# Performance work log

Hardware: AMD Instinct MI355X
Metric: run time of the kernel (lower is better)

Reference implementation:

```python
import jax, jax.numpy as jnp
import numpy as np

N_NODES = 50000


def _gcn_conv(h, W, b, src, dst, dinv):
    # PyG GCNConv: linear transform, then symmetric-normalized sum aggregation
    h = h @ W  # (N, d_out)
    norm = dinv[src] * dinv[dst]  # (E,)
    msg = h[src] * norm[:, None]  # (E, d_out)
    agg = jax.ops.segment_sum(msg, dst, num_segments=N_NODES)
    return agg + b


def setup_inputs() -> dict:
    key = jax.random.key(0)
    ks = jax.random.split(key, 9)
    in_dim, h1, h2, out_dim = 512, 512, 512, 256
    x = jax.random.normal(ks[0], (N_NODES, in_dim), dtype=jnp.float32)
    edge_index = jax.random.randint(ks[1], (2, 800000), 0, N_NODES, dtype=jnp.int64)

    def glorot(k, shape):
        lim = float(np.sqrt(6.0 / (shape[0] + shape[1])))
        return jax.random.uniform(k, shape, jnp.float32, -lim, lim)

    return {
        "x": x,
        "edge_index": edge_index,
        "W1": glorot(ks[2], (in_dim, h1)),
        "b1": jnp.zeros((h1,), jnp.float32),
        "W2": glorot(ks[3], (h1, h2)),
        "b2": jnp.zeros((h2,), jnp.float32),
        "Wout": glorot(ks[4], (h2, out_dim)),
        "bout": jnp.zeros((out_dim,), jnp.float32),
    }


def reference(x, edge_index, W1, b1, W2, b2, Wout, bout):
    # add self-loops (GCNConv default)
    loop = jnp.arange(N_NODES, dtype=edge_index.dtype)
    src = jnp.concatenate([edge_index[0], loop])
    dst = jnp.concatenate([edge_index[1], loop])
    # degree on A + I (target side), deg^{-1/2}
    deg = jax.ops.segment_sum(jnp.ones_like(dst, dtype=x.dtype), dst, num_segments=N_NODES)
    dinv = jnp.where(deg > 0, jax.lax.rsqrt(deg), 0.0)

    h = jax.nn.relu(_gcn_conv(x, W1, b1, src, dst, dinv))
    h = jax.nn.relu(_gcn_conv(h, W2, b2, src, dst, dinv))
    return h @ Wout + bout
```

## Files before the change

kernel.cpp:

```cpp
#include <hip/hip_runtime.h>

#define NN 50000
#define MP 50048
#define DD 512
#define EE 800000
#define NSCAN 196

typedef unsigned short u16;
typedef __attribute__((ext_vector_type(4))) float f32x4;
typedef __attribute__((ext_vector_type(8))) __bf16 bf16x8;
typedef __attribute__((ext_vector_type(8))) short s16x8;
typedef __attribute__((ext_vector_type(4))) short s16x4;

typedef __attribute__((address_space(1))) const void GVoid;
typedef __attribute__((address_space(3))) void LVoid;

__device__ __forceinline__ u16 f2bf(float f) {
  union { float f; unsigned u; } x; x.f = f;
  unsigned r = x.u + 0x7fffu + ((x.u >> 16) & 1u);
  return (u16)(r >> 16);
}
__device__ __forceinline__ float bf2f(u16 b) {
  union { unsigned u; float f; } x; x.u = ((unsigned)b) << 16;
  return x.f;
}


__global__ __launch_bounds__(256) void init_cnt_k(int* cnt) {
  int i = blockIdx.x * 256 + threadIdx.x;
  if (i < NN) cnt[i] = 1;
}

__global__ __launch_bounds__(256) void count_k(const int* __restrict__ dst, int* __restrict__ cnt) {
  int e = blockIdx.x * 256 + threadIdx.x;
  if (e < EE) atomicAdd(&cnt[dst[e]], 1);
}

__global__ __launch_bounds__(256) void dinv_k(const int* __restrict__ cnt, float* __restrict__ dinv) {
  int i = blockIdx.x * 256 + threadIdx.x;
  if (i < NN) dinv[i] = rsqrtf((float)cnt[i]);
}


__global__ __launch_bounds__(256) void scan1_k(const int* __restrict__ cnt, int* __restrict__ bsum) {
  __shared__ int s[256];
  const int t = threadIdx.x;
  const int i = blockIdx.x * 256 + t;
  s[t] = (i < NN) ? cnt[i] : 0;
  __syncthreads();
  for (int off = 128; off > 0; off >>= 1) {
    if (t < off) s[t] += s[t + off];
    __syncthreads();
  }
  if (t == 0) bsum[blockIdx.x] = s[0];
}

__global__ __launch_bounds__(256) void scan2_k(const int* __restrict__ bsum, int* __restrict__ boff) {
  __shared__ int s[256];
  const int t = threadIdx.x;
  const int v = (t < NSCAN) ? bsum[t] : 0;
  s[t] = v;
  __syncthreads();
  for (int off = 1; off < 256; off <<= 1) {
    int a = s[t];
    int b = (t >= off) ? s[t - off] : 0;
    __syncthreads();
    s[t] = a + b;
    __syncthreads();
  }
  if (t < NSCAN) boff[t] = s[t] - v;
}

__global__ __launch_bounds__(256) void scan3_k(const int* __restrict__ cnt, const int* __restrict__ boff,
                                               int* __restrict__ rowp, int* __restrict__ cursor) {
  __shared__ int s[256];
  const int t = threadIdx.x;
  const int i = blockIdx.x * 256 + t;
  const int v = (i < NN) ? cnt[i] : 0;
  s[t] = v;
  __syncthreads();
  for (int off = 1; off < 256; off <<= 1) {
    int a = s[t];
    int b = (t >= off) ? s[t - off] : 0;
    __syncthreads();
    s[t] = a + b;
    __syncthreads();
  }
  const int excl = s[t] - v + boff[blockIdx.x];
  if (i < NN) { rowp[i] = excl; cursor[i] = excl; }
  if (i == NN - 1) rowp[NN] = excl + v;
}

__global__ __launch_bounds__(256) void scatter_k(const int* __restrict__ src, const int* __restrict__ dst,
                                                 const float* __restrict__ dinv, int* __restrict__ cursor,
                                                 int2* __restrict__ csr) {
  int e = blockIdx.x * 256 + threadIdx.x;
  if (e < EE) {
    int d = dst[e], s = src[e];
    int pos = atomicAdd(&cursor[d], 1);
    csr[pos] = make_int2(s, __float_as_int(dinv[s] * dinv[d]));
  } else if (e < EE + NN) {
    int i = e - EE;
    int pos = atomicAdd(&cursor[i], 1);
    float di = dinv[i];
    csr[pos] = make_int2(i, __float_as_int(di * di));
  }
}


__global__ __launch_bounds__(256) void convert_x_k(const float* __restrict__ x, u16* __restrict__ xb) {
  size_t i = ((size_t)blockIdx.x * 256 + threadIdx.x) * 4;
  if (i >= (size_t)MP * DD) return;
  s16x4 v;
  if (i < (size_t)NN * DD) {
    f32x4 f = *(const f32x4*)(x + i);
    v = (s16x4){ (short)f2bf(f.x), (short)f2bf(f.y), (short)f2bf(f.z), (short)f2bf(f.w) };
  } else {
    v = (s16x4){ 0, 0, 0, 0 };
  }
  *(s16x4*)(xb + i) = v;
}

__global__ __launch_bounds__(256) void convert_wt_k(const float* __restrict__ W, u16* __restrict__ WT, int ncols) {
  int idx = blockIdx.x * 256 + threadIdx.x;
  if (idx >= 512 * ncols) return;
  int n = idx >> 9, k = idx & 511;
  WT[idx] = f2bf(W[(size_t)k * ncols + n]);
}


template<int OUT_BF16>
__global__ __launch_bounds__(256) void gemm_k(const u16* __restrict__ A, const u16* __restrict__ BT,
                                              void* __restrict__ Cv, const float* __restrict__ bias,
                                              int M, int N) {
  const int nwg = (int)gridDim.x;
  const int id = (int)blockIdx.x;
  const int xcd = id & 7;
  const int idx = id >> 3;
  const int q = nwg >> 3, r = nwg & 7;
  const int tile = (xcd < r ? xcd * (q + 1) : r * (q + 1) + (xcd - r) * q) + idx;
  const int ntn = N >> 7;
  const int bm = tile / ntn;
  const int bn = tile % ntn;

  __shared__ u16 As[2][128 * 32];
  __shared__ u16 Bs[2][128 * 32];
  const int t = threadIdx.x;
  const int lane = t & 63;
  const int wc = (t >> 6) & 1;
  const int wr = (t >> 7) & 1;
  f32x4 acc[4][4] = {};
  const int r0 = t >> 2;
  const int kc = (t & 3) * 8;
  const u16* Ab = A + (size_t)bm * 128 * DD + (size_t)r0 * DD + kc;
  const u16* Bb = BT + (size_t)bn * 128 * DD + (size_t)r0 * DD + kc;

  auto stage = [&](int buf, int kt) {
    __builtin_amdgcn_global_load_lds((GVoid*)(Ab + kt),           (LVoid*)(&As[buf][t * 8]),        16, 0, 0);
    __builtin_amdgcn_global_load_lds((GVoid*)(Ab + 64 * DD + kt), (LVoid*)(&As[buf][2048 + t * 8]), 16, 0, 0);
    __builtin_amdgcn_global_load_lds((GVoid*)(Bb + kt),           (LVoid*)(&Bs[buf][t * 8]),        16, 0, 0);
    __builtin_amdgcn_global_load_lds((GVoid*)(Bb + 64 * DD + kt), (LVoid*)(&Bs[buf][2048 + t * 8]), 16, 0, 0);
  };

  stage(0, 0);
  __syncthreads();

  #pragma unroll 2
  for (int step = 0; step < 16; ++step) {
    const int cur = step & 1;
    if (step < 15) stage(cur ^ 1, (step + 1) * 32);
    bf16x8 af[4], bv[4];
    #pragma unroll
    for (int m = 0; m < 4; ++m)
      af[m] = *(const bf16x8*)&As[cur][(wr * 64 + m * 16 + (lane & 15)) * 32 + (lane >> 4) * 8];
    #pragma unroll
    for (int n = 0; n < 4; ++n)
      bv[n] = *(const bf16x8*)&Bs[cur][(wc * 64 + n * 16 + (lane & 15)) * 32 + (lane >> 4) * 8];
    #pragma unroll
    for (int m = 0; m < 4; ++m) {
      #pragma unroll
      for (int n = 0; n < 4; ++n)
        acc[m][n] = __builtin_amdgcn_mfma_f32_16x16x32_bf16(af[m], bv[n], acc[m][n], 0, 0, 0);
    }
    __syncthreads();
  }

  const int rb = bm * 128 + wr * 64 + ((lane >> 4) * 4);
  const int cb = bn * 128 + wc * 64 + (lane & 15);
  #pragma unroll
  for (int m = 0; m < 4; ++m) {
    #pragma unroll
    for (int rr = 0; rr < 4; ++rr) {
      const int row = rb + m * 16 + rr;
      if (row < M) {
        #pragma unroll
        for (int n = 0; n < 4; ++n) {
          const int col = cb + n * 16;
          float v = acc[m][n][rr];
          if (bias) v += bias[col];
          if (OUT_BF16) ((u16*)Cv)[(size_t)row * N + col] = f2bf(v);
          else          ((float*)Cv)[(size_t)row * N + col] = v;
        }
      }
    }
  }
}


__global__ __launch_bounds__(256) void aggregate_k(const u16* __restrict__ H, const int* __restrict__ rowp,
                                                   const int2* __restrict__ csr,
                                                   const float* __restrict__ bias,
                                                   u16* __restrict__ out) {
  const int wid = threadIdx.x >> 6;
  const int lane = threadIdx.x & 63;
  const int node = blockIdx.x * 4 + wid;
  const int d0 = lane * 8;
  const int beg = rowp[node];
  const int end = rowp[node + 1];
  float acc[8] = {0.f, 0.f, 0.f, 0.f, 0.f, 0.f, 0.f, 0.f};
  int e = beg;
  for (; e + 4 <= end; e += 4) {
    const int2 c0 = csr[e], c1 = csr[e + 1], c2 = csr[e + 2], c3 = csr[e + 3];
    const s16x8 v0 = *(const s16x8*)(H + (size_t)c0.x * DD + d0);
    const s16x8 v1 = *(const s16x8*)(H + (size_t)c1.x * DD + d0);
    const s16x8 v2 = *(const s16x8*)(H + (size_t)c2.x * DD + d0);
    const s16x8 v3 = *(const s16x8*)(H + (size_t)c3.x * DD + d0);
    const float w0 = __int_as_float(c0.y), w1 = __int_as_float(c1.y);
    const float w2 = __int_as_float(c2.y), w3 = __int_as_float(c3.y);
    #pragma unroll
    for (int j = 0; j < 8; ++j) {
      acc[j] += bf2f((u16)v0[j]) * w0;
      acc[j] += bf2f((u16)v1[j]) * w1;
      acc[j] += bf2f((u16)v2[j]) * w2;
      acc[j] += bf2f((u16)v3[j]) * w3;
    }
  }
  for (; e < end; ++e) {
    const int2 c = csr[e];
    const s16x8 v = *(const s16x8*)(H + (size_t)c.x * DD + d0);
    const float w = __int_as_float(c.y);
    #pragma unroll
    for (int j = 0; j < 8; ++j) acc[j] += bf2f((u16)v[j]) * w;
  }
  s16x8 o;
  #pragma unroll
  for (int j = 0; j < 8; ++j) {
    float r = acc[j] + bias[d0 + j];
    r = fmaxf(r, 0.f);
    o[j] = (short)f2bf(r);
  }
  *(s16x8*)(out + (size_t)node * DD + d0) = o;
}


extern "C" void kernel_launch(void* const* d_in, const int* in_sizes, int n_in,
                              void* d_out, int out_size, void* d_ws, size_t ws_size,
                              hipStream_t stream) {
  const float* x    = (const float*)d_in[0];
  const int*   ei   = (const int*)d_in[1];
  const float* W1   = (const float*)d_in[2];
  const float* b1   = (const float*)d_in[3];
  const float* W2   = (const float*)d_in[4];
  const float* b2   = (const float*)d_in[5];
  const float* Wout = (const float*)d_in[6];
  const float* bout = (const float*)d_in[7];
  float* out = (float*)d_out;
  (void)in_sizes; (void)n_in; (void)out_size; (void)ws_size;

  char* ws = (char*)d_ws;
  size_t off = 0;
  auto alloc = [&](size_t bytes) -> char* {
    char* p = ws + off;
    off = (off + bytes + 255) & ~(size_t)255;
    return p;
  };
  u16*   xb   = (u16*)alloc((size_t)MP * DD * 2);
  u16*   H    = (u16*)alloc((size_t)NN * DD * 2);
  u16*   W1T  = (u16*)alloc(512 * 512 * 2);
  u16*   W2T  = (u16*)alloc(512 * 512 * 2);
  u16*   WoT  = (u16*)alloc(256 * 512 * 2);
  int*   cnt  = (int*)alloc(NN * 4);
  float* dinv = (float*)alloc(NN * 4);
  int*   rowp = (int*)alloc((NN + 1) * 4);
  int*   cur  = (int*)alloc(NN * 4);
  int2*  csr  = (int2*)alloc((size_t)(EE + NN) * 8);
  int*   bsum = (int*)alloc(NSCAN * 4);
  int*   boff = (int*)alloc(NSCAN * 4);

  const int* srcp = ei;
  const int* dstp = ei + EE;

  init_cnt_k<<<(NN + 255) / 256, 256, 0, stream>>>(cnt);
  count_k<<<(EE + 255) / 256, 256, 0, stream>>>(dstp, cnt);
  dinv_k<<<(NN + 255) / 256, 256, 0, stream>>>(cnt, dinv);
  scan1_k<<<NSCAN, 256, 0, stream>>>(cnt, bsum);
  scan2_k<<<1, 256, 0, stream>>>(bsum, boff);
  scan3_k<<<NSCAN, 256, 0, stream>>>(cnt, boff, rowp, cur);
  scatter_k<<<(EE + NN + 255) / 256, 256, 0, stream>>>(srcp, dstp, dinv, cur, csr);
  convert_x_k<<<(int)(((size_t)MP * DD / 4 + 255) / 256), 256, 0, stream>>>(x, xb);
  convert_wt_k<<<(512 * 512 + 255) / 256, 256, 0, stream>>>(W1, W1T, 512);
  convert_wt_k<<<(512 * 512 + 255) / 256, 256, 0, stream>>>(W2, W2T, 512);
  convert_wt_k<<<(512 * 256 + 255) / 256, 256, 0, stream>>>(Wout, WoT, 256);

  gemm_k<1><<<(MP / 128) * (512 / 128), 256, 0, stream>>>(xb, W1T, (void*)H, nullptr, NN, 512);
  aggregate_k<<<NN / 4, 256, 0, stream>>>(H, rowp, csr, b1, xb);
  gemm_k<1><<<(MP / 128) * (512 / 128), 256, 0, stream>>>(xb, W2T, (void*)H, nullptr, NN, 512);
  aggregate_k<<<NN / 4, 256, 0, stream>>>(H, rowp, csr, b2, xb);
  gemm_k<0><<<(MP / 128) * (256 / 128), 256, 0, stream>>>(xb, WoT, (void*)out, bout, NN, 256);
}
```

Before: 500.1 us.

## Fuse fp32-to-bf16 conversion into first GEMM and merge setup kernels

The separate x-to-bf16 conversion kernel is removed. The first GEMM now loads fp32 X directly, converts it in registers and writes it to LDS, which avoids a full write and re-read of the bf16 copy of x. The CSR scatter is folded into the same launch as extra leading blocks, dinv is computed inside scan3, and the count init is merged with the weight transposes, cutting several launches. In exchange, the A-operand path now goes through registers instead of direct global-to-LDS loads, and the scatter blocks share the grid with the GEMM tiles.

```diff
diff --git a/kernel.cpp b/kernel.cpp
--- a/kernel.cpp
+++ b/kernel.cpp
@@ -5,12 +5,13 @@
 #define DD 512
 #define EE 800000
 #define NSCAN 196
+#define SCB 3321
+#define G1TILES 1564
 
 typedef unsigned short u16;
 typedef __attribute__((ext_vector_type(4))) float f32x4;
 typedef __attribute__((ext_vector_type(8))) __bf16 bf16x8;
 typedef __attribute__((ext_vector_type(8))) short s16x8;
-typedef __attribute__((ext_vector_type(4))) short s16x4;
 
 typedef __attribute__((address_space(1))) const void GVoid;
 typedef __attribute__((address_space(3))) void LVoid;
@@ -26,9 +27,19 @@
 }
 
 
-__global__ __launch_bounds__(256) void init_cnt_k(int* cnt) {
-  int i = blockIdx.x * 256 + threadIdx.x;
-  if (i < NN) cnt[i] = 1;
+__global__ __launch_bounds__(256) void setup_k(int* __restrict__ cnt,
+                                               const float* __restrict__ W1, u16* __restrict__ W1T,
+                                               const float* __restrict__ W2, u16* __restrict__ W2T,
+                                               const float* __restrict__ Wo, u16* __restrict__ WoT) {
+  const int b = (int)blockIdx.x, t = threadIdx.x;
+  if (b < 196) { int i = b * 256 + t; if (i < NN) cnt[i] = 1; return; }
+  const float* W; u16* WT; int ncols, idx;
+  if (b < 1220)      { W = W1; WT = W1T; ncols = 512; idx = (b - 196) * 256 + t; }
+  else if (b < 2244) { W = W2; WT = W2T; ncols = 512; idx = (b - 1220) * 256 + t; }
+  else               { W = Wo; WT = WoT; ncols = 256; idx = (b - 2244) * 256 + t; }
+  if (idx >= 512 * ncols) return;
+  int n = idx >> 9, k = idx & 511;
+  WT[idx] = f2bf(W[(size_t)k * ncols + n]);
 }
 
 __global__ __launch_bounds__(256) void count_k(const int* __restrict__ dst, int* __restrict__ cnt) {
@@ -36,11 +47,6 @@
   if (e < EE) atomicAdd(&cnt[dst[e]], 1);
 }
 
-__global__ __launch_bounds__(256) void dinv_k(const int* __restrict__ cnt, float* __restrict__ dinv) {
-  int i = blockIdx.x * 256 + threadIdx.x;
-  if (i < NN) dinv[i] = rsqrtf((float)cnt[i]);
-}
-
 
 __global__ __launch_bounds__(256) void scan1_k(const int* __restrict__ cnt, int* __restrict__ bsum) {
   __shared__ int s[256];
@@ -72,7 +78,8 @@
 }
 
 __global__ __launch_bounds__(256) void scan3_k(const int* __restrict__ cnt, const int* __restrict__ boff,
-                                               int* __restrict__ rowp, int* __restrict__ cursor) {
+                                               int* __restrict__ rowp, int* __restrict__ cursor,
+                                               float* __restrict__ dinv) {
   __shared__ int s[256];
   const int t = threadIdx.x;
   const int i = blockIdx.x * 256 + t;
@@ -87,45 +94,119 @@
     __syncthreads();
   }
   const int excl = s[t] - v + boff[blockIdx.x];
-  if (i < NN) { rowp[i] = excl; cursor[i] = excl; }
+  if (i < NN) {
+    rowp[i] = excl; cursor[i] = excl;
+    dinv[i] = rsqrtf((float)v);
+  }
   if (i == NN - 1) rowp[NN] = excl + v;
 }
 
-__global__ __launch_bounds__(256) void scatter_k(const int* __restrict__ src, const int* __restrict__ dst,
-                                                 const float* __restrict__ dinv, int* __restrict__ cursor,
-                                                 int2* __restrict__ csr) {
-  int e = blockIdx.x * 256 + threadIdx.x;
-  if (e < EE) {
-    int d = dst[e], s = src[e];
-    int pos = atomicAdd(&cursor[d], 1);
-    csr[pos] = make_int2(s, __float_as_int(dinv[s] * dinv[d]));
-  } else if (e < EE + NN) {
-    int i = e - EE;
-    int pos = atomicAdd(&cursor[i], 1);
-    float di = dinv[i];
-    csr[pos] = make_int2(i, __float_as_int(di * di));
-  }
-}
-
-
-__global__ __launch_bounds__(256) void convert_x_k(const float* __restrict__ x, u16* __restrict__ xb) {
-  size_t i = ((size_t)blockIdx.x * 256 + threadIdx.x) * 4;
-  if (i >= (size_t)MP * DD) return;
-  s16x4 v;
-  if (i < (size_t)NN * DD) {
-    f32x4 f = *(const f32x4*)(x + i);
-    v = (s16x4){ (short)f2bf(f.x), (short)f2bf(f.y), (short)f2bf(f.z), (short)f2bf(f.w) };
-  } else {
-    v = (s16x4){ 0, 0, 0, 0 };
-  }
-  *(s16x4*)(xb + i) = v;
-}
-
-__global__ __launch_bounds__(256) void convert_wt_k(const float* __restrict__ W, u16* __restrict__ WT, int ncols) {
-  int idx = blockIdx.x * 256 + threadIdx.x;
-  if (idx >= 512 * ncols) return;
-  int n = idx >> 9, k = idx & 511;
-  WT[idx] = f2bf(W[(size_t)k * ncols + n]);
+
+__global__ __launch_bounds__(256) void gemm1_k(const float* __restrict__ X, const u16* __restrict__ BT,
+                                               u16* __restrict__ C,
+                                               const int* __restrict__ src, const int* __restrict__ dst,
+                                               const float* __restrict__ dinv, int* __restrict__ cursor,
+                                               int2* __restrict__ csr) {
+  __shared__ u16 As[2][128 * 32];
+  __shared__ u16 Bs[2][128 * 32];
+  const int t = threadIdx.x;
+
+  if (blockIdx.x < SCB) {
+    int e = (int)blockIdx.x * 256 + t;
+    if (e < EE) {
+      int d = dst[e], sn = src[e];
+      int pos = atomicAdd(&cursor[d], 1);
+      csr[pos] = make_int2(sn, __float_as_int(dinv[sn] * dinv[d]));
+    } else if (e < EE + NN) {
+      int i = e - EE;
+      int pos = atomicAdd(&cursor[i], 1);
+      float di = dinv[i];
+      csr[pos] = make_int2(i, __float_as_int(di * di));
+    }
+    return;
+  }
+
+  const int g = (int)blockIdx.x - SCB;
+  const int xcd = g & 7;
+  const int idx = g >> 3;
+  const int q = G1TILES >> 3, r = G1TILES & 7;
+  const int tile = (xcd < r ? xcd * (q + 1) : r * (q + 1) + (xcd - r) * q) + idx;
+  const int bm = tile >> 2;
+  const int bn = tile & 3;
+
+  const int lane = t & 63;
+  const int wc = (t >> 6) & 1;
+  const int wr = (t >> 7) & 1;
+  f32x4 acc[4][4] = {};
+  const int r0 = t >> 2;
+  const int kc = (t & 3) * 8;
+  const int row1 = bm * 128 + 64 + r0;
+  const float* Xp0 = X + (size_t)(bm * 128 + r0) * DD + kc;
+  const float* Xp1 = X + (size_t)(row1 < NN ? row1 : NN - 1) * DD + kc;
+  const u16* Bb = BT + (size_t)bn * 128 * DD + (size_t)r0 * DD + kc;
+
+  f32x4 a0, a1, a2, a3;
+  auto loadA = [&](int kt) {
+    a0 = *(const f32x4*)(Xp0 + kt);
+    a1 = *(const f32x4*)(Xp0 + kt + 4);
+    a2 = *(const f32x4*)(Xp1 + kt);
+    a3 = *(const f32x4*)(Xp1 + kt + 4);
+  };
+  auto writeA = [&](int buf) {
+    bf16x8 w0, w1;
+    #pragma unroll
+    for (int j = 0; j < 4; ++j) {
+      w0[j] = (__bf16)a0[j]; w0[4 + j] = (__bf16)a1[j];
+      w1[j] = (__bf16)a2[j]; w1[4 + j] = (__bf16)a3[j];
+    }
+    *(bf16x8*)&As[buf][t * 8] = w0;
+    *(bf16x8*)&As[buf][2048 + t * 8] = w1;
+  };
+  auto stageB = [&](int buf, int kt) {
+    __builtin_amdgcn_global_load_lds((GVoid*)(Bb + kt),           (LVoid*)(&Bs[buf][t * 8]),        16, 0, 0);
+    __builtin_amdgcn_global_load_lds((GVoid*)(Bb + 64 * DD + kt), (LVoid*)(&Bs[buf][2048 + t * 8]), 16, 0, 0);
+  };
+
+  loadA(0);
+  stageB(0, 0);
+  writeA(0);
+  __syncthreads();
+
+  #pragma unroll 2
+  for (int step = 0; step < 16; ++step) {
+    const int cur = step & 1;
+    if (step < 15) { loadA((step + 1) * 32); stageB(cur ^ 1, (step + 1) * 32); }
+    bf16x8 af[4], bv[4];
+    #pragma unroll
+    for (int m = 0; m < 4; ++m)
+      af[m] = *(const bf16x8*)&As[cur][(wr * 64 + m * 16 + (lane & 15)) * 32 + (lane >> 4) * 8];
+    #pragma unroll
+    for (int n = 0; n < 4; ++n)
+      bv[n] = *(const bf16x8*)&Bs[cur][(wc * 64 + n * 16 + (lane & 15)) * 32 + (lane >> 4) * 8];
+    #pragma unroll
+    for (int m = 0; m < 4; ++m) {
+      #pragma unroll
+      for (int n = 0; n < 4; ++n)
+        acc[m][n] = __builtin_amdgcn_mfma_f32_16x16x32_bf16(af[m], bv[n], acc[m][n], 0, 0, 0);
+    }
+    if (step < 15) writeA(cur ^ 1);
+    __syncthreads();
+  }
+
+  const int rb = bm * 128 + wr * 64 + ((lane >> 4) * 4);
+  const int cb = bn * 128 + wc * 64 + (lane & 15);
+  #pragma unroll
+  for (int m = 0; m < 4; ++m) {
+    #pragma unroll
+    for (int rr = 0; rr < 4; ++rr) {
+      const int row = rb + m * 16 + rr;
+      if (row < NN) {
+        #pragma unroll
+        for (int n = 0; n < 4; ++n)
+          C[(size_t)row * 512 + cb + n * 16] = f2bf(acc[m][n][rr]);
+      }
+    }
+  }
 }
 
 
@@ -290,19 +371,13 @@
   const int* srcp = ei;
   const int* dstp = ei + EE;
 
-  init_cnt_k<<<(NN + 255) / 256, 256, 0, stream>>>(cnt);
+  setup_k<<<2756, 256, 0, stream>>>(cnt, W1, W1T, W2, W2T, Wout, WoT);
   count_k<<<(EE + 255) / 256, 256, 0, stream>>>(dstp, cnt);
-  dinv_k<<<(NN + 255) / 256, 256, 0, stream>>>(cnt, dinv);
   scan1_k<<<NSCAN, 256, 0, stream>>>(cnt, bsum);
   scan2_k<<<1, 256, 0, stream>>>(bsum, boff);
-  scan3_k<<<NSCAN, 256, 0, stream>>>(cnt, boff, rowp, cur);
-  scatter_k<<<(EE + NN + 255) / 256, 256, 0, stream>>>(srcp, dstp, dinv, cur, csr);
-  convert_x_k<<<(int)(((size_t)MP * DD / 4 + 255) / 256), 256, 0, stream>>>(x, xb);
-  convert_wt_k<<<(512 * 512 + 255) / 256, 256, 0, stream>>>(W1, W1T, 512);
-  convert_wt_k<<<(512 * 512 + 255) / 256, 256, 0, stream>>>(W2, W2T, 512);
-  convert_wt_k<<<(512 * 256 + 255) / 256, 256, 0, stream>>>(Wout, WoT, 256);
-
-  gemm_k<1><<<(MP / 128) * (512 / 128), 256, 0, stream>>>(xb, W1T, (void*)H, nullptr, NN, 512);
+  scan3_k<<<NSCAN, 256, 0, stream>>>(cnt, boff, rowp, cur, dinv);
+
+  gemm1_k<<<SCB + G1TILES, 256, 0, stream>>>(x, W1T, H, srcp, dstp, dinv, cur, csr);
   aggregate_k<<<NN / 4, 256, 0, stream>>>(H, rowp, csr, b1, xb);
   gemm_k<1><<<(MP / 128) * (512 / 128), 256, 0, stream>>>(xb, W2T, (void*)H, nullptr, NN, 512);
   aggregate_k<<<NN / 4, 256, 0, stream>>>(H, rowp, csr, b2, xb);
```

Measured after the change: 478.6 us. 4.3% less time.
